# Kernel optimization log

Measured on AMD Instinct MI355X. Metric: run time of the kernel, lower is better.

The kernel has to match this reference:

```python
import jax, jax.numpy as jnp
import numpy as np

SEQ, BATCH, HID = 4096, 32, 512


def setup_inputs() -> dict:
    key = jax.random.key(0)
    ks = jax.random.split(key, 7)
    s = 1.0 / np.sqrt(HID)
    return {
        "x0": jax.random.normal(ks[0], (SEQ, BATCH, 1), dtype=jnp.float32),
        "W_ih": jax.random.uniform(ks[1], (4 * HID, 1), jnp.float32, -s, s),
        "W_hh": jax.random.uniform(ks[2], (4 * HID, HID), jnp.float32, -s, s),
        "b_ih": jax.random.uniform(ks[3], (4 * HID,), jnp.float32, -s, s),
        "b_hh": jax.random.uniform(ks[4], (4 * HID,), jnp.float32, -s, s),
        "W_lin": jax.random.uniform(ks[5], (1, HID), jnp.float32, -s, s),
        "b_lin": jax.random.uniform(ks[6], (1,), jnp.float32, -s, s),
    }


def _lstm(x0, W_ih, W_hh, b_ih, b_hh):
    # x0: (T, B, 1). Precompute input contribution to gates for all steps.
    x_proj = jnp.einsum("tbi,gi->tbg", x0, W_ih) + (b_ih + b_hh)  # (T, B, 4H)
    T, B, _ = x_proj.shape
    H = W_hh.shape[1]
    h0 = jnp.zeros((B, H), x0.dtype)
    c0 = jnp.zeros((B, H), x0.dtype)

    def step(carry, xp):
        h, c = carry
        gates = xp + h @ W_hh.T  # (B, 4H)
        i, f, g, o = jnp.split(gates, 4, axis=-1)  # torch gate order i,f,g,o
        i = jax.nn.sigmoid(i)
        f = jax.nn.sigmoid(f)
        g = jnp.tanh(g)
        o = jax.nn.sigmoid(o)
        c = f * c + i * g
        h = o * jnp.tanh(c)
        return (h, c), h

    _, hs = jax.lax.scan(step, (h0, c0), x_proj)  # hs: (T, B, H)
    return hs


def reference(x0, W_ih, W_hh, b_ih, b_hh, W_lin, b_lin):
    hs = _lstm(x0, W_ih, W_hh, b_ih, b_hh)            # (T, B, H)
    y = jnp.einsum("tbh,oh->tbo", hs, W_lin) + b_lin  # (T, B, 1)
    return y + x0                                      # residual add
```

## Files before the change

kernel.cpp:

```cpp
#include <hip/hip_runtime.h>
#include <stdint.h>

#define T_STEPS 4096
#define BATCH 32
#define HID 512
#define GROUPS 8
#define BLK_THREADS 1024
#define NBLOCKS 256

typedef _Float16 h2_t __attribute__((ext_vector_type(2)));
typedef uint32_t u32x16 __attribute__((ext_vector_type(16)));

__device__ inline uint32_t pack_h2(float a, float b) {
  h2_t v;
  v.x = (_Float16)a;
  v.y = (_Float16)b;
  return __builtin_bit_cast(uint32_t, v);
}

__device__ inline float fdot2(uint32_t a, uint32_t b, float c) {
  return __builtin_amdgcn_fdot2(__builtin_bit_cast(h2_t, a),
                                __builtin_bit_cast(h2_t, b), c, false);
}

__device__ inline uint32_t aread(uint32_t a) {
  uint32_t v;
  asm("v_accvgpr_read_b32 %0, %1" : "=v"(v) : "a"(a));
  return v;
}

__device__ inline uint64_t uni64(const void* p) {
  uint32_t lo = __builtin_amdgcn_readfirstlane((uint32_t)(uintptr_t)p);
  uint32_t hi = __builtin_amdgcn_readfirstlane((uint32_t)((uintptr_t)p >> 32));
  return ((uint64_t)hi << 32) | lo;
}

__device__ inline void kinv() {
  asm volatile("s_dcache_inv" ::: "memory");
}
__device__ inline uint32_t sload1(uint64_t p) {
  uint32_t v;
  asm volatile("s_load_dword %0, %1, 0x0\n\ts_waitcnt lgkmcnt(0)"
               : "=s"(v) : "s"(p) : "memory");
  return v;
}
__device__ inline u32x16 sload16(uint64_t p) {
  u32x16 v;
  asm volatile("s_load_dwordx16 %0, %1, 0x0\n\ts_waitcnt lgkmcnt(0)"
               : "=s"(v) : "s"(p) : "memory");
  return v;
}
__device__ inline void waitcnt_vm0() {
  asm volatile("s_waitcnt vmcnt(0)" ::: "memory");
}

__device__ inline float sigf(float x) { return 1.0f / (1.0f + __expf(-x)); }
__device__ inline float tanh_fast(float x) {
  float a = fabsf(x);
  float e = __expf(-2.0f * a);
  float r = (1.0f - e) / (1.0f + e);
  return copysignf(r, x);
}

__global__ __launch_bounds__(BLK_THREADS)
void lstm_smem(const float* __restrict__ x0,
               const float* __restrict__ W_ih,
               const float* __restrict__ W_hh,
               const float* __restrict__ b_ih,
               const float* __restrict__ b_hh,
               const float* __restrict__ W_lin,
               const float* __restrict__ b_lin,
               float* __restrict__ y,
               uint32_t* __restrict__ h_ex,
               uint32_t* __restrict__ cnt,
               int* __restrict__ claim)
{
  __shared__ float x0_lds[T_STEPS];
  __shared__ float ylds[T_STEPS];
  __shared__ float gacc[2][256];
  __shared__ int s_bg;

  const int tid = threadIdx.x;

  if (tid == 0) {
    uint32_t xcc;
    asm volatile("s_getreg_b32 %0, hwreg(HW_REG_XCC_ID)" : "=s"(xcc));
    xcc &= 7;
    int slot = atomicAdd(claim + xcc * 16, 1);
    s_bg = (slot < 32) ? (int)(((4 * xcc + (slot >> 3)) << 3) | (slot & 7))
                       : -1;
  }
  __syncthreads();
  if (s_bg < 0) return;
  const int b  = s_bg >> 3;
  const int g  = s_bg & 7;
  const int u0 = g * 64;
  const int wv = tid >> 6;
  const int rg = wv >> 3;
  const int cs = wv & 7;
  const int l  = tid & 63;

  uint32_t a0[32], a1[32];
  {
    const int r0 = 128 * rg + l;
    const int r1 = r0 + 64;
    const int R0 = (r0 >> 6) * HID + u0 + (r0 & 63);
    const int R1 = (r1 >> 6) * HID + u0 + (r1 & 63);
    const float2* p0 = (const float2*)(W_hh + (size_t)R0 * HID + 64 * cs);
    const float2* p1 = (const float2*)(W_hh + (size_t)R1 * HID + 64 * cs);
#pragma unroll
    for (int k = 0; k < 32; ++k) {
      float2 a = p0[k], c = p1[k];
      uint32_t t0 = pack_h2(a.x, a.y);
      uint32_t t1 = pack_h2(c.x, c.y);
      asm("v_accvgpr_write_b32 %0, %1" : "=a"(a0[k]) : "v"(t0));
      asm("v_accvgpr_write_b32 %0, %1" : "=a"(a1[k]) : "v"(t1));
    }
  }
  for (int i = tid; i < T_STEPS; i += BLK_THREADS) {
    x0_lds[i] = x0[i * BATCH + b];
    ylds[i] = 0.f;
  }
  if (tid < 256) { gacc[0][tid] = 0.f; gacc[1][tid] = 0.f; }

  float c_state = 0.f;
  float wih_[4] = {0.f, 0.f, 0.f, 0.f}, bs_[4] = {0.f, 0.f, 0.f, 0.f};
  float wlin_u = 0.f, blin = 0.f;
  if (tid < 64) {
#pragma unroll
    for (int j = 0; j < 4; ++j) {
      int R = j * HID + u0 + tid;
      wih_[j] = W_ih[R];
      bs_[j] = b_ih[R] + b_hh[R];
    }
    wlin_u = W_lin[u0 + tid];
    blin = b_lin[0];
  }

  uint32_t* hb = h_ex + (size_t)b * 256;
  const uint64_t dpu[2] = { uni64(hb + 32 * cs),
                            uni64(hb + BATCH * 256 + 32 * cs) };
  const uint64_t cwu = uni64(cnt + b * 16 + cs);
  uint32_t* pub01[2] = { hb + 32 * g, hb + BATCH * 256 + 32 * g };
  uint32_t* cnt_b = cnt + b * 16;

  __syncthreads();

  int dead = 0;
  for (int t = 0; t < T_STEPS; ++t) {
    const int sl = t & 1, ns = sl ^ 1;

    {
      int guard = 0;
      for (;;) {
        kinv();
        uint32_t c = sload1(cwu);
        if ((int)c >= t) break;
        if (dead || ++guard > (1 << 20)) { dead = 1; break; }
        __builtin_amdgcn_s_sleep(1);
      }
    }
    u32x16 hs0 = sload16(dpu[sl]);
    u32x16 hs1 = sload16(dpu[sl] + 64);

    float acc0 = 0.f, acc1 = 0.f;
#pragma unroll
    for (int k = 0; k < 16; ++k) {
      acc0 = fdot2(aread(a0[k]), hs0[k], acc0);
      acc1 = fdot2(aread(a1[k]), hs0[k], acc1);
    }
#pragma unroll
    for (int k = 0; k < 16; ++k) {
      acc0 = fdot2(aread(a0[16 + k]), hs1[k], acc0);
      acc1 = fdot2(aread(a1[16 + k]), hs1[k], acc1);
    }
    atomicAdd(&gacc[sl][128 * rg + l], acc0);
    atomicAdd(&gacc[sl][128 * rg + 64 + l], acc1);
    __syncthreads();

    if (tid < 64) {
      const float xv = x0_lds[t];
      float gi = gacc[sl][tid]       + xv * wih_[0] + bs_[0];
      float gf = gacc[sl][tid + 64]  + xv * wih_[1] + bs_[1];
      float gg = gacc[sl][tid + 128] + xv * wih_[2] + bs_[2];
      float go = gacc[sl][tid + 192] + xv * wih_[3] + bs_[3];
      float si = sigf(gi), sf = sigf(gf), tg_ = tanh_fast(gg), so = sigf(go);
      c_state = sf * c_state + si * tg_;
      float h = so * tanh_fast(c_state);

      float hn = __shfl_down(h, 1, 64);
      if ((tid & 1) == 0) pub01[ns][tid >> 1] = pack_h2(h, hn);
      waitcnt_vm0();
      if (tid == 0) cnt_b[g] = (uint32_t)(t + 1);

      gacc[sl][tid] = 0.f;
      gacc[sl][tid + 64] = 0.f;
      gacc[sl][tid + 128] = 0.f;
      gacc[sl][tid + 192] = 0.f;

      float p = wlin_u * h;
#pragma unroll
      for (int m = 32; m >= 1; m >>= 1) p += __shfl_xor(p, m, 64);
      if (tid == 0) ylds[t] = p;
    }
  }

  __syncthreads();
  for (int i = tid; i < T_STEPS; i += BLK_THREADS) {
    float val = ylds[i];
    if (g == 0) val += blin + x0_lds[i];
    unsafeAtomicAdd(&y[i * BATCH + b], val);
  }
}

extern "C" void kernel_launch(void* const* d_in, const int* in_sizes, int n_in,
                              void* d_out, int out_size, void* d_ws, size_t ws_size,
                              hipStream_t stream) {
  const float* x0    = (const float*)d_in[0];
  const float* W_ih  = (const float*)d_in[1];
  const float* W_hh  = (const float*)d_in[2];
  const float* b_ih  = (const float*)d_in[3];
  const float* b_hh  = (const float*)d_in[4];
  const float* W_lin = (const float*)d_in[5];
  const float* b_lin = (const float*)d_in[6];
  float* y = (float*)d_out;

  uint32_t* h_ex = (uint32_t*)d_ws;
  uint32_t* cnt  = h_ex + 2 * BATCH * 256;
  int* claim     = (int*)(cnt + BATCH * 16);
  const size_t init_bytes = (2 * BATCH * 256 + BATCH * 16) * sizeof(uint32_t)
                            + 8 * 16 * sizeof(int);

  (void)hipMemsetAsync(d_ws, 0, init_bytes, stream);
  (void)hipMemsetAsync(d_out, 0, (size_t)out_size * sizeof(float), stream);

  hipLaunchKernelGGL(lstm_smem, dim3(NBLOCKS), dim3(BLK_THREADS), 0, stream,
                     x0, W_ih, W_hh, b_ih, b_hh, W_lin, b_lin, y, h_ex, cnt,
                     claim);
}
```

Baseline: 14.97 ms.

## Replace counter-based handoff with step-tagged hidden-state words

Each hidden value is now published as a 32-bit word holding the fp16 value in the low half and the step number in the high half. Consumers poll the data itself with four scalar x16 loads and check every tag, instead of waiting on a separate counter and then loading the data. This removes the producer's vmcnt wait before the counter store and one dependent round trip per step. In exchange the exchange buffer doubles in size, each poll reads 256 bytes, and the fp16 pairs must be repacked before the dot products.

Result: slower. 16.04 ms (+7.2%).

```diff
diff --git a/kernel.cpp b/kernel.cpp
--- a/kernel.cpp
+++ b/kernel.cpp
@@ -38,20 +38,16 @@
 __device__ inline void kinv() {
   asm volatile("s_dcache_inv" ::: "memory");
 }
-__device__ inline uint32_t sload1(uint64_t p) {
-  uint32_t v;
-  asm volatile("s_load_dword %0, %1, 0x0\n\ts_waitcnt lgkmcnt(0)"
-               : "=s"(v) : "s"(p) : "memory");
-  return v;
-}
-__device__ inline u32x16 sload16(uint64_t p) {
-  u32x16 v;
-  asm volatile("s_load_dwordx16 %0, %1, 0x0\n\ts_waitcnt lgkmcnt(0)"
-               : "=s"(v) : "s"(p) : "memory");
-  return v;
-}
-__device__ inline void waitcnt_vm0() {
-  asm volatile("s_waitcnt vmcnt(0)" ::: "memory");
+__device__ inline void sload64(uint64_t p, u32x16& h0, u32x16& h1,
+                               u32x16& h2, u32x16& h3) {
+  asm volatile(
+      "s_load_dwordx16 %0, %4, 0x0\n\t"
+      "s_load_dwordx16 %1, %4, 0x40\n\t"
+      "s_load_dwordx16 %2, %4, 0x80\n\t"
+      "s_load_dwordx16 %3, %4, 0xc0\n\t"
+      "s_waitcnt lgkmcnt(0)"
+      : "=s"(h0), "=s"(h1), "=s"(h2), "=s"(h3)
+      : "s"(p) : "memory");
 }
 
 __device__ inline float sigf(float x) { return 1.0f / (1.0f + __expf(-x)); }
@@ -63,17 +59,16 @@
 }
 
 __global__ __launch_bounds__(BLK_THREADS)
-void lstm_smem(const float* __restrict__ x0,
-               const float* __restrict__ W_ih,
-               const float* __restrict__ W_hh,
-               const float* __restrict__ b_ih,
-               const float* __restrict__ b_hh,
-               const float* __restrict__ W_lin,
-               const float* __restrict__ b_lin,
-               float* __restrict__ y,
-               uint32_t* __restrict__ h_ex,
-               uint32_t* __restrict__ cnt,
-               int* __restrict__ claim)
+void lstm_tag(const float* __restrict__ x0,
+              const float* __restrict__ W_ih,
+              const float* __restrict__ W_hh,
+              const float* __restrict__ b_ih,
+              const float* __restrict__ b_hh,
+              const float* __restrict__ W_lin,
+              const float* __restrict__ b_lin,
+              float* __restrict__ y,
+              uint32_t* __restrict__ h_ex,
+              int* __restrict__ claim)
 {
   __shared__ float x0_lds[T_STEPS];
   __shared__ float ylds[T_STEPS];
@@ -137,12 +132,10 @@
     blin = b_lin[0];
   }
 
-  uint32_t* hb = h_ex + (size_t)b * 256;
-  const uint64_t dpu[2] = { uni64(hb + 32 * cs),
-                            uni64(hb + BATCH * 256 + 32 * cs) };
-  const uint64_t cwu = uni64(cnt + b * 16 + cs);
-  uint32_t* pub01[2] = { hb + 32 * g, hb + BATCH * 256 + 32 * g };
-  uint32_t* cnt_b = cnt + b * 16;
+  uint32_t* hb = h_ex + (size_t)b * 512;
+  const uint64_t dpu[2] = { uni64(hb + 64 * cs),
+                            uni64(hb + BATCH * 512 + 64 * cs) };
+  uint32_t* pub01[2] = { hb + u0 + tid, hb + BATCH * 512 + u0 + tid };
 
   __syncthreads();
 
@@ -150,29 +143,36 @@
   for (int t = 0; t < T_STEPS; ++t) {
     const int sl = t & 1, ns = sl ^ 1;
 
+    u32x16 h0, h1, h2, h3;
     {
+      const uint32_t tw = (uint32_t)t << 16;
       int guard = 0;
       for (;;) {
         kinv();
-        uint32_t c = sload1(cwu);
-        if ((int)c >= t) break;
+        sload64(dpu[sl], h0, h1, h2, h3);
+        uint32_t bad = 0;
+#pragma unroll
+        for (int k = 0; k < 16; ++k) {
+          bad |= (h0[k] ^ tw) | (h1[k] ^ tw) | (h2[k] ^ tw) | (h3[k] ^ tw);
+        }
+        if ((bad & 0xffff0000u) == 0u) break;
         if (dead || ++guard > (1 << 20)) { dead = 1; break; }
         __builtin_amdgcn_s_sleep(1);
       }
     }
-    u32x16 hs0 = sload16(dpu[sl]);
-    u32x16 hs1 = sload16(dpu[sl] + 64);
-
+    uint32_t pk[32];
+#pragma unroll
+    for (int e = 0; e < 8; ++e) {
+      pk[e]      = (h0[2 * e] & 0xffffu) | (h0[2 * e + 1] << 16);
+      pk[8 + e]  = (h1[2 * e] & 0xffffu) | (h1[2 * e + 1] << 16);
+      pk[16 + e] = (h2[2 * e] & 0xffffu) | (h2[2 * e + 1] << 16);
+      pk[24 + e] = (h3[2 * e] & 0xffffu) | (h3[2 * e + 1] << 16);
+    }
     float acc0 = 0.f, acc1 = 0.f;
 #pragma unroll
-    for (int k = 0; k < 16; ++k) {
-      acc0 = fdot2(aread(a0[k]), hs0[k], acc0);
-      acc1 = fdot2(aread(a1[k]), hs0[k], acc1);
-    }
-#pragma unroll
-    for (int k = 0; k < 16; ++k) {
-      acc0 = fdot2(aread(a0[16 + k]), hs1[k], acc0);
-      acc1 = fdot2(aread(a1[16 + k]), hs1[k], acc1);
+    for (int k = 0; k < 32; ++k) {
+      acc0 = fdot2(aread(a0[k]), pk[k], acc0);
+      acc1 = fdot2(aread(a1[k]), pk[k], acc1);
     }
     atomicAdd(&gacc[sl][128 * rg + l], acc0);
     atomicAdd(&gacc[sl][128 * rg + 64 + l], acc1);
@@ -188,10 +188,8 @@
       c_state = sf * c_state + si * tg_;
       float h = so * tanh_fast(c_state);
 
-      float hn = __shfl_down(h, 1, 64);
-      if ((tid & 1) == 0) pub01[ns][tid >> 1] = pack_h2(h, hn);
-      waitcnt_vm0();
-      if (tid == 0) cnt_b[g] = (uint32_t)(t + 1);
+      uint16_t hbb = __builtin_bit_cast(uint16_t, (_Float16)h);
+      pub01[ns][0] = ((uint32_t)(t + 1) << 16) | (uint32_t)hbb;
 
       gacc[sl][tid] = 0.f;
       gacc[sl][tid + 64] = 0.f;
@@ -226,15 +224,13 @@
   float* y = (float*)d_out;
 
   uint32_t* h_ex = (uint32_t*)d_ws;
-  uint32_t* cnt  = h_ex + 2 * BATCH * 256;
-  int* claim     = (int*)(cnt + BATCH * 16);
-  const size_t init_bytes = (2 * BATCH * 256 + BATCH * 16) * sizeof(uint32_t)
-                            + 8 * 16 * sizeof(int);
+  int* claim = (int*)(h_ex + 2 * BATCH * 512);
+  const size_t init_bytes =
+      (size_t)2 * BATCH * 512 * sizeof(uint32_t) + 8 * 16 * sizeof(int);
 
   (void)hipMemsetAsync(d_ws, 0, init_bytes, stream);
   (void)hipMemsetAsync(d_out, 0, (size_t)out_size * sizeof(float), stream);
 
-  hipLaunchKernelGGL(lstm_smem, dim3(NBLOCKS), dim3(BLK_THREADS), 0, stream,
-                     x0, W_ih, W_hh, b_ih, b_hh, W_lin, b_lin, y, h_ex, cnt,
-                     claim);
-}
+  hipLaunchKernelGGL(lstm_tag, dim3(NBLOCKS), dim3(BLK_THREADS), 0, stream,
+                     x0, W_ih, W_hh, b_ih, b_hh, W_lin, b_lin, y, h_ex, claim);
+}
```
